# Kernel optimization log

Hardware: AMD Instinct MI355X
Metric: run time of the kernel (lower is better)

## Reference

```python
import jax, jax.numpy as jnp
import numpy as np

IN_DIMS = 4
DEPTH = 4
C = IN_DIMS + 1                     # channels after time augmentation
SIG = sum(C ** k for k in range(1, DEPTH + 1))  # 780
N, T = 64, 1024


def setup_inputs() -> dict:
    key = jax.random.key(0)
    k1, k2, k3, k4, k5 = jax.random.split(key, 5)
    batch = jax.random.normal(k1, (N, T, IN_DIMS), dtype=jnp.float32)
    s_c = 1.0 / np.sqrt(C)
    conv_w = jax.random.normal(k2, (C, C), dtype=jnp.float32) * s_c
    conv_b = jax.random.normal(k3, (C,), dtype=jnp.float32) * s_c
    s_l = 1.0 / np.sqrt(SIG)
    lin_w = jax.random.normal(k4, (SIG, SIG), dtype=jnp.float32) * s_l
    lin_b = jax.random.normal(k5, (SIG,), dtype=jnp.float32) * s_l
    return {"batch": batch, "conv_w": conv_w, "conv_b": conv_b,
            "lin_w": lin_w, "lin_b": lin_b}


def _stream_signature(path):
    """Streamed path signature with zero basepoint.

    path: (n, t, C). Returns (n, t, SIG) where entry t is the signature of
    the piecewise-linear path (0, path[0], ..., path[t]) truncated at DEPTH,
    levels flattened in lexicographic (row-major) order like signatory.
    """
    n = path.shape[0]
    # increments; basepoint=True means first increment is path[:,0] - 0
    dx = jnp.concatenate([path[:, :1, :], path[:, 1:, :] - path[:, :-1, :]], axis=1)
    init = tuple(jnp.zeros((n, C ** k), path.dtype) for k in range(1, DEPTH + 1))

    def step(levels, d):
        # exp(d) in the truncated tensor algebra: e_k = d^{(x)k} / k!
        e = [d]
        for k in range(2, DEPTH + 1):
            e.append((jnp.einsum('na,nb->nab', e[-1], d) / k).reshape(n, -1))
        # Chen: new_k = e_k + S_k + sum_{i=1}^{k-1} S_i (x) e_{k-i}
        new = []
        for k in range(1, DEPTH + 1):
            acc = levels[k - 1] + e[k - 1]
            for i in range(1, k):
                acc = acc + jnp.einsum('na,nb->nab', levels[i - 1], e[k - i - 1]).reshape(n, -1)
            new.append(acc)
        new = tuple(new)
        return new, jnp.concatenate(new, axis=-1)

    _, ys = jax.lax.scan(step, init, jnp.swapaxes(dx, 0, 1))  # ys: (t, n, SIG)
    return jnp.swapaxes(ys, 0, 1)


def reference(batch, conv_w, conv_b, lin_w, lin_b):
    n, t, _ = batch.shape
    # time augmentation: append channel arange(1,T+1)/T
    time = (jnp.arange(1, t + 1, dtype=batch.dtype) / t)[None, :, None]
    a = jnp.concatenate([batch, jnp.broadcast_to(time, (n, t, 1))], axis=-1)  # (n,t,C)
    # kernel-size-1 conv1d == pointwise linear over channels
    b = a @ conv_w.T + conv_b                                                  # (n,t,C)
    c = _stream_signature(b)                                                   # (n,t,SIG)
    # zero out the first stream entry (torch.concat of zeros with c[:,1:,:])
    c = jnp.concatenate([jnp.zeros((n, 1, SIG), c.dtype), c[:, 1:, :]], axis=1)
    return jnp.tanh(c @ lin_w.T + lin_b)
```

## Files before the change

kernel.cpp:

```cpp
#include <hip/hip_runtime.h>
#include <math.h>

#define N_B 64
#define T_LEN 1024
#define IN_D 4
#define CH 5
#define SIG 780
#define KP 800
#define SEG_LEN 16
#define N_SEG 64
#define SC_L1 1.0f
#define SC_L2 0.25f
#define SC_L3 0.0625f
#define SC_L4 0.015625f

typedef _Float16 f16x8 __attribute__((ext_vector_type(8)));
typedef float f32x4 __attribute__((ext_vector_type(4)));

typedef __attribute__((address_space(1))) const void* as1cp;
typedef __attribute__((address_space(3))) void* as3p;

__device__ __forceinline__ float fast_tanh(float x) {
  float ax = fabsf(x);
  float e = __expf(-2.0f * ax);
  float r = (1.0f - e) * __builtin_amdgcn_rcpf(1.0f + e);
  return copysignf(r, x);
}

__global__ __launch_bounds__(256) void conv_kernel(
    const float* __restrict__ batch,
    const float* __restrict__ conv_w,
    const float* __restrict__ conv_b,
    float* __restrict__ b_out) {
  int idx = blockIdx.x * blockDim.x + threadIdx.x;
  if (idx >= N_B * T_LEN) return;
  int t = idx & (T_LEN - 1);
  const float* a = batch + (size_t)idx * IN_D;
  float a0 = a[0], a1 = a[1], a2 = a[2], a3 = a[3];
  float tm = (float)(t + 1) / (float)T_LEN;
  float* o = b_out + (size_t)idx * CH;
#pragma unroll
  for (int j = 0; j < CH; ++j) {
    const float* w = conv_w + j * CH;
    float r = conv_b[j];
    r = fmaf(tm, w[4], r);
    r = fmaf(a3, w[3], r);
    r = fmaf(a2, w[2], r);
    r = fmaf(a1, w[1], r);
    r = fmaf(a0, w[0], r);
    o[j] = r;
  }
}

__global__ __launch_bounds__(320) void seg_kernel(
    const float* __restrict__ batch,
    const float* __restrict__ conv_w,
    const float* __restrict__ conv_b,
    float* __restrict__ P) {
  int s = blockIdx.x;
  int n = blockIdx.y;
  int tid = threadIdx.x;

  __shared__ float S[SIG];
  __shared__ float bc[(SEG_LEN + 1) * CH];
  __shared__ float dsh[SEG_LEN][CH];

  for (int i = tid; i < SIG; i += 320) S[i] = 0.0f;
  if (tid < (SEG_LEN + 1) * CH) {
    int r = s * SEG_LEN - 1 + tid / CH, ch = tid % CH;
    float v = 0.0f;
    if (r >= 0) {
      const float* a = batch + ((size_t)n * T_LEN + r) * IN_D;
      const float* w = conv_w + ch * CH;
      v = conv_b[ch];
      v = fmaf(a[0], w[0], v);
      v = fmaf(a[1], w[1], v);
      v = fmaf(a[2], w[2], v);
      v = fmaf(a[3], w[3], v);
      v = fmaf((float)(r + 1) * (1.0f / T_LEN), w[4], v);
    }
    bc[tid] = v;
  }
  __syncthreads();
  if (tid < SEG_LEN * CH) {
    int j = tid / CH, ch = tid % CH;
    dsh[j][ch] = bc[(j + 1) * CH + ch] - bc[j * CH + ch];
  }

  const int x0 = tid;
  const int x1 = tid + 320;
  const bool has1 = (tid < 305);
  const int a0i = x0 / 125, b0i = (x0 / 25) % 5, c0i = (x0 / 5) % 5, d0i = x0 % 5;
  const int a1i = x1 / 125, b1i = (x1 / 25) % 5, c1i = (x1 / 5) % 5, d1i = x1 % 5;
  const int s2_0 = x0 / 25, s3_0 = x0 / 5;
  const int s2_1 = x1 / 25, s3_1 = x1 / 5;
  const bool hasL3 = (tid < 125);
  const int ya = tid / 25, yb = (tid / 5) % 5, yc = tid % 5;
  const bool hasL2 = (tid < 25);
  const int za = tid / 5, zb = tid % 5;
  const bool hasL1 = (tid < CH);
  __syncthreads();

  for (int j = 0; j < SEG_LEN; ++j) {
    float n4_0, n4_1 = 0.0f, n3 = 0.0f, n2 = 0.0f, n1 = 0.0f;
    {
      float tH = fmaf(0.25f, dsh[j][a0i], S[a0i]);
      tH = fmaf((1.0f / 3.0f) * dsh[j][b0i], tH, S[5 + s2_0]);
      tH = fmaf(0.5f * dsh[j][c0i], tH, S[30 + s3_0]);
      n4_0 = fmaf(dsh[j][d0i], tH, S[155 + x0]);
    }
    if (has1) {
      float tH = fmaf(0.25f, dsh[j][a1i], S[a1i]);
      tH = fmaf((1.0f / 3.0f) * dsh[j][b1i], tH, S[5 + s2_1]);
      tH = fmaf(0.5f * dsh[j][c1i], tH, S[30 + s3_1]);
      n4_1 = fmaf(dsh[j][d1i], tH, S[155 + x1]);
    }
    if (hasL3) {
      float tH = fmaf((1.0f / 3.0f), dsh[j][ya], S[ya]);
      tH = fmaf(0.5f * dsh[j][yb], tH, S[5 + ya * 5 + yb]);
      n3 = fmaf(dsh[j][yc], tH, S[30 + tid]);
    }
    if (hasL2) {
      float tH = fmaf(0.5f, dsh[j][za], S[za]);
      n2 = fmaf(dsh[j][zb], tH, S[5 + tid]);
    }
    if (hasL1) n1 = S[tid] + dsh[j][tid];
    __syncthreads();
    S[155 + x0] = n4_0;
    if (has1) S[155 + x1] = n4_1;
    if (hasL3) S[30 + tid] = n3;
    if (hasL2) S[5 + tid] = n2;
    if (hasL1) S[tid] = n1;
    __syncthreads();
  }

  float* Pr = P + ((size_t)n * N_SEG + s) * SIG;
  for (int i = tid; i < SIG; i += 320) Pr[i] = S[i];
}

__global__ __launch_bounds__(640) void prefix_kernel(float* __restrict__ P) {
  int n = blockIdx.x;
  int tid = threadIdx.x;
  __shared__ float A[SIG];
  __shared__ float Bs[SIG];

  float* Pn = P + (size_t)n * N_SEG * SIG;
  for (int i = tid; i < SIG; i += 640) A[i] = Pn[i];
  int i0 = tid, i1 = tid + 640;
  float r0 = 0.f, r1 = 0.f;
  if (i0 < SIG) r0 = Pn[SIG + i0];
  if (i1 < SIG) r1 = Pn[SIG + i1];

  const int e4 = tid;
  const int q4a = e4 / 125, r125 = e4 % 125, r25 = e4 % 25, r5 = e4 % 5;
  const int e4d5 = e4 / 5, e4d25 = e4 / 25;
  const int e3 = tid;
  const int e3a = e3 / 25, e3r25 = e3 % 25, e3r5 = e3 % 5, e3d5 = e3 / 5;
  const int e2 = tid - 125;
  const int e1 = tid - 150;

  for (int s = 1; s < N_SEG; ++s) {
    if (i0 < SIG) Bs[i0] = r0;
    if (i1 < SIG) Bs[i1] = r1;
    __syncthreads();
    if (s + 1 < N_SEG) {
      const float* Pnx = Pn + (size_t)(s + 1) * SIG;
      if (i0 < SIG) r0 = Pnx[i0];
      if (i1 < SIG) r1 = Pnx[i1];
    }
    float v4 = 0.f, v3 = 0.f, v2 = 0.f, v1 = 0.f;
    if (tid < 625) {
      v4 = A[155 + e4] + Bs[155 + e4];
      v4 = fmaf(A[30 + e4d5], Bs[r5], v4);
      v4 = fmaf(A[5 + e4d25], Bs[5 + r25], v4);
      v4 = fmaf(A[q4a], Bs[30 + r125], v4);
    }
    if (tid < 125) {
      v3 = A[30 + e3] + Bs[30 + e3];
      v3 = fmaf(A[5 + e3d5], Bs[e3r5], v3);
      v3 = fmaf(A[e3a], Bs[5 + e3r25], v3);
    } else if (tid < 150) {
      v2 = A[5 + e2] + Bs[5 + e2];
      v2 = fmaf(A[e2 / 5], Bs[e2 % 5], v2);
    } else if (tid < 155) {
      v1 = A[e1] + Bs[e1];
    }
    __syncthreads();
    float* Po = Pn + (size_t)s * SIG;
    if (tid < 625) { A[155 + e4] = v4; Po[155 + e4] = v4; }
    if (tid < 125) { A[30 + e3] = v3; Po[30 + e3] = v3; }
    else if (tid < 150) { A[5 + e2] = v2; Po[5 + e2] = v2; }
    else if (tid < 155) { A[e1] = v1; Po[e1] = v1; }
  }
}

__global__ __launch_bounds__(320) void emit_kernel(
    const float* __restrict__ batch,
    const float* __restrict__ conv_w,
    const float* __restrict__ conv_b,
    const float* __restrict__ P,
    _Float16* __restrict__ c1,
    _Float16* __restrict__ c2) {
  int s = blockIdx.x;
  int n = blockIdx.y;
  int tid = threadIdx.x;

  __shared__ float S[SIG];
  __shared__ float bc[(SEG_LEN + 1) * CH];
  __shared__ float dsh[SEG_LEN][CH];
  __shared__ __align__(16) _Float16 row1[KP];
  __shared__ __align__(16) _Float16 row2[KP];

  if (s == 0) {
    for (int i = tid; i < SIG; i += 320) S[i] = 0.0f;
  } else {
    const float* Pr = P + ((size_t)n * N_SEG + (s - 1)) * SIG;
    for (int i = tid; i < SIG; i += 320) S[i] = Pr[i];
  }
  if (tid < (SEG_LEN + 1) * CH) {
    int r = s * SEG_LEN - 1 + tid / CH, ch = tid % CH;
    float v = 0.0f;
    if (r >= 0) {
      const float* a = batch + ((size_t)n * T_LEN + r) * IN_D;
      const float* w = conv_w + ch * CH;
      v = conv_b[ch];
      v = fmaf(a[0], w[0], v);
      v = fmaf(a[1], w[1], v);
      v = fmaf(a[2], w[2], v);
      v = fmaf(a[3], w[3], v);
      v = fmaf((float)(r + 1) * (1.0f / T_LEN), w[4], v);
    }
    bc[tid] = v;
  }
  if (tid < KP - SIG) {
    row1[SIG + tid] = (_Float16)0.0f;
    row2[SIG + tid] = (_Float16)0.0f;
  }
  __syncthreads();
  if (tid < SEG_LEN * CH) {
    int j = tid / CH, ch = tid % CH;
    dsh[j][ch] = bc[(j + 1) * CH + ch] - bc[j * CH + ch];
  }

  const int x0 = tid;
  const int x1 = tid + 320;
  const bool has1 = (tid < 305);
  const int a0i = x0 / 125, b0i = (x0 / 25) % 5, c0i = (x0 / 5) % 5, d0i = x0 % 5;
  const int a1i = x1 / 125, b1i = (x1 / 25) % 5, c1i = (x1 / 5) % 5, d1i = x1 % 5;
  const int s2_0 = x0 / 25, s3_0 = x0 / 5;
  const int s2_1 = x1 / 25, s3_1 = x1 / 5;
  const bool hasL3 = (tid < 125);
  const int ya = tid / 25, yb = (tid / 5) % 5, yc = tid % 5;
  const bool hasL2 = (tid < 25);
  const int za = tid / 5, zb = tid % 5;
  const bool hasL1 = (tid < CH);
  __syncthreads();

  for (int j = 0; j < SEG_LEN; ++j) {
    int t = s * SEG_LEN + j;
    float n4_0, n4_1 = 0.0f, n3 = 0.0f, n2 = 0.0f, n1 = 0.0f;
    {
      float tH = fmaf(0.25f, dsh[j][a0i], S[a0i]);
      tH = fmaf((1.0f / 3.0f) * dsh[j][b0i], tH, S[5 + s2_0]);
      tH = fmaf(0.5f * dsh[j][c0i], tH, S[30 + s3_0]);
      n4_0 = fmaf(dsh[j][d0i], tH, S[155 + x0]);
    }
    if (has1) {
      float tH = fmaf(0.25f, dsh[j][a1i], S[a1i]);
      tH = fmaf((1.0f / 3.0f) * dsh[j][b1i], tH, S[5 + s2_1]);
      tH = fmaf(0.5f * dsh[j][c1i], tH, S[30 + s3_1]);
      n4_1 = fmaf(dsh[j][d1i], tH, S[155 + x1]);
    }
    if (hasL3) {
      float tH = fmaf((1.0f / 3.0f), dsh[j][ya], S[ya]);
      tH = fmaf(0.5f * dsh[j][yb], tH, S[5 + ya * 5 + yb]);
      n3 = fmaf(dsh[j][yc], tH, S[30 + tid]);
    }
    if (hasL2) {
      float tH = fmaf(0.5f, dsh[j][za], S[za]);
      n2 = fmaf(dsh[j][zb], tH, S[5 + tid]);
    }
    if (hasL1) n1 = S[tid] + dsh[j][tid];
    __syncthreads();

    S[155 + x0] = n4_0;
    if (has1) S[155 + x1] = n4_1;
    if (hasL3) S[30 + tid] = n3;
    if (hasL2) S[5 + tid] = n2;
    if (hasL1) S[tid] = n1;

    float z = (t == 0) ? 0.0f : 1.0f;
    {
      float v = n4_0 * SC_L4 * z;
      _Float16 h = (_Float16)v;
      row1[155 + x0] = h; row2[155 + x0] = (_Float16)(v - (float)h);
    }
    if (has1) {
      float v = n4_1 * SC_L4 * z;
      _Float16 h = (_Float16)v;
      row1[155 + x1] = h; row2[155 + x1] = (_Float16)(v - (float)h);
    }
    if (hasL3) {
      float v = n3 * SC_L3 * z;
      _Float16 h = (_Float16)v;
      row1[30 + tid] = h; row2[30 + tid] = (_Float16)(v - (float)h);
    }
    if (hasL2) {
      float v = n2 * SC_L2 * z;
      _Float16 h = (_Float16)v;
      row1[5 + tid] = h; row2[5 + tid] = (_Float16)(v - (float)h);
    }
    if (hasL1) {
      float v = n1 * SC_L1 * z;
      _Float16 h = (_Float16)v;
      row1[tid] = h; row2[tid] = (_Float16)(v - (float)h);
    }
    __syncthreads();

    size_t base = ((size_t)n * T_LEN + t) * KP;
    if (tid < 100) {
      *(float4*)(c1 + base + tid * 8) = *(const float4*)&row1[tid * 8];
    } else if (tid < 200) {
      int c = tid - 100;
      *(float4*)(c2 + base + c * 8) = *(const float4*)&row2[c * 8];
    }
  }
}

__global__ __launch_bounds__(256) void wconv_kernel(
    const float* __restrict__ W,
    _Float16* __restrict__ w1,
    _Float16* __restrict__ w2) {
  int idx = blockIdx.x * blockDim.x + threadIdx.x;
  if (idx >= 896 * KP) return;
  int nn = idx / KP, k = idx % KP;
  float v = 0.0f;
  if (nn < SIG && k < SIG) {
    float sc = (k < 5) ? 1.0f : (k < 30) ? 4.0f : (k < 155) ? 16.0f : 64.0f;
    v = W[(size_t)nn * SIG + k] * sc;
  }
  _Float16 h = (_Float16)v;
  w1[idx] = h;
  w2[idx] = (_Float16)(v - (float)h);
}

__global__ __launch_bounds__(256) void gemm_mfma(
    const _Float16* __restrict__ A1p, const _Float16* __restrict__ A2p,
    const _Float16* __restrict__ B1p, const _Float16* __restrict__ B2p,
    const float* __restrict__ bias, float* __restrict__ out) {
  __shared__ _Float16 Al[2][2][128 * 32];
  __shared__ _Float16 Bl[2][2][128 * 32];

  int tid = threadIdx.x;
  int lane = tid & 63, wid = tid >> 6;
  int wm = wid >> 1, wn = wid & 1;
  int m0 = blockIdx.y * 128;
  int n0 = blockIdx.x * 128;

  f32x4 acc[4][4];
#pragma unroll
  for (int i = 0; i < 4; ++i)
#pragma unroll
    for (int j = 0; j < 4; ++j) acc[i][j] = (f32x4){0.f, 0.f, 0.f, 0.f};

  int sr = lane >> 2, scn = lane & 3;
  int swst = (sr ^ (sr >> 2)) & 3;
  int qg = scn ^ swst;
  int fr = lane & 15, fq = lane >> 4;
  int swf = (fr ^ (fr >> 2)) & 3;
  int fchunk = fq ^ swf;

  auto stage = [&](int kb, int buf) {
    int k0 = kb * 32;
#pragma unroll
    for (int i = 0; i < 2; ++i) {
      int rloc = wid * 16 + i * 64 + sr;
      size_t gA = (size_t)(m0 + rloc) * KP + k0 + qg * 8;
      size_t gB = (size_t)(n0 + rloc) * KP + k0 + qg * 8;
      int lb = (wid * 16 + i * 64) * 32;
      __builtin_amdgcn_global_load_lds((as1cp)(A1p + gA), (as3p)(&Al[buf][0][lb]), 16, 0, 0);
      __builtin_amdgcn_global_load_lds((as1cp)(A2p + gA), (as3p)(&Al[buf][1][lb]), 16, 0, 0);
      __builtin_amdgcn_global_load_lds((as1cp)(B1p + gB), (as3p)(&Bl[buf][0][lb]), 16, 0, 0);
      __builtin_amdgcn_global_load_lds((as1cp)(B2p + gB), (as3p)(&Bl[buf][1][lb]), 16, 0, 0);
    }
  };

  stage(0, 0);
  for (int kb = 0; kb < 25; ++kb) {
    int cur = kb & 1;
    __syncthreads();
    f16x8 a1[4], a2[4], b1[4], b2[4];
#pragma unroll
    for (int tm = 0; tm < 4; ++tm) {
      int off = (wm * 64 + tm * 16 + fr) * 32 + fchunk * 8;
      a1[tm] = *(const f16x8*)&Al[cur][0][off];
      a2[tm] = *(const f16x8*)&Al[cur][1][off];
    }
#pragma unroll
    for (int tn = 0; tn < 4; ++tn) {
      int off = (wn * 64 + tn * 16 + fr) * 32 + fchunk * 8;
      b1[tn] = *(const f16x8*)&Bl[cur][0][off];
      b2[tn] = *(const f16x8*)&Bl[cur][1][off];
    }
    if (kb < 24) stage(kb + 1, cur ^ 1);
#pragma unroll
    for (int tm = 0; tm < 4; ++tm)
#pragma unroll
      for (int tn = 0; tn < 4; ++tn) {
        acc[tm][tn] = __builtin_amdgcn_mfma_f32_16x16x32_f16(a1[tm], b1[tn], acc[tm][tn], 0, 0, 0);
        acc[tm][tn] = __builtin_amdgcn_mfma_f32_16x16x32_f16(a1[tm], b2[tn], acc[tm][tn], 0, 0, 0);
        acc[tm][tn] = __builtin_amdgcn_mfma_f32_16x16x32_f16(a2[tm], b1[tn], acc[tm][tn], 0, 0, 0);
      }
  }
  __syncthreads();

  float* ep = (float*)((wid < 2) ? (void*)&Al[0][0][0] : (void*)&Bl[0][0][0]);
  ep += (wid & 1) * 4096;

  float bv[4];
#pragma unroll
  for (int tn = 0; tn < 4; ++tn) {
    int nn = n0 + wn * 64 + tn * 16 + fr;
    bv[tn] = (nn < SIG) ? bias[nn] : 0.0f;
  }
#pragma unroll
  for (int h = 0; h < 2; ++h) {
#pragma unroll
    for (int tm2 = 0; tm2 < 2; ++tm2) {
      int tm = h * 2 + tm2;
#pragma unroll
      for (int tn = 0; tn < 4; ++tn) {
#pragma unroll
        for (int r = 0; r < 4; ++r) {
          int lr = tm2 * 16 + fq * 4 + r;
          int lc = tn * 16 + fr;
          ep[lr * 66 + lc] = fast_tanh(acc[tm][tn][r] + bv[tn]);
        }
      }
    }
#pragma unroll
    for (int p = 0; p < 2; ++p) {
      int lr = lane & 31;
      int ck = (lane >> 5) * 2 + p;
      int gm = m0 + wm * 64 + h * 32 + lr;
      int gc0 = n0 + wn * 64 + ck * 16;
#pragma unroll
      for (int q = 0; q < 4; ++q) {
        int col = gc0 + q * 4;
        if (col + 3 < SIG) {
          *(float4*)(out + (size_t)gm * SIG + col) =
              *(const float4*)&ep[lr * 66 + ck * 16 + q * 4];
        } else if (col < SIG) {
#pragma unroll
          for (int e = 0; e < 4; ++e) {
            int c2 = col + e;
            if (c2 < SIG) out[(size_t)gm * SIG + c2] = ep[lr * 66 + ck * 16 + q * 4 + e];
          }
        }
      }
    }
  }
}

__global__ __launch_bounds__(320) void sig_kernel_fb(
    const float* __restrict__ b_in, float* __restrict__ c_out) {
  int n = blockIdx.x;
  int tid = threadIdx.x;
  __shared__ float S[SIG];
  __shared__ float bc[64 * CH];
  __shared__ float dsh[CH];
  __shared__ float pb[CH];
  for (int i = tid; i < SIG; i += 320) S[i] = 0.0f;
  if (tid < CH) pb[tid] = 0.0f;
  const float* bn = b_in + (size_t)n * T_LEN * CH;
  float* cn = c_out + (size_t)n * T_LEN * SIG;
  const int x0 = tid, x1 = tid + 320;
  const bool has1 = (tid < 305);
  const int a0i = x0 / 125, b0i = (x0 / 25) % 5, c0i = (x0 / 5) % 5, d0i = x0 % 5;
  const int a1i = x1 / 125, b1i = (x1 / 25) % 5, c1i = (x1 / 5) % 5, d1i = x1 % 5;
  const int s2_0 = x0 / 25, s3_0 = x0 / 5, s2_1 = x1 / 25, s3_1 = x1 / 5;
  const bool hasL3 = (tid < 125);
  const int ya = tid / 25, yb = (tid / 5) % 5, yc = tid % 5;
  const bool hasL2 = (tid < 25);
  const int za = tid / 5, zb = tid % 5;
  const bool hasL1 = (tid < CH);
  for (int t = 0; t < T_LEN; ++t) {
    if ((t & 63) == 0) {
      __syncthreads();
      bc[tid] = bn[t * CH + tid];
      __syncthreads();
    }
    if (tid < CH) {
      float cur = bc[(t & 63) * CH + tid];
      dsh[tid] = cur - pb[tid];
      pb[tid] = cur;
    }
    __syncthreads();
    float n4_0, n4_1 = 0.0f, n3 = 0.0f, n2 = 0.0f, n1 = 0.0f;
    {
      float tH = fmaf(0.25f, dsh[a0i], S[a0i]);
      tH = fmaf((1.0f / 3.0f) * dsh[b0i], tH, S[5 + s2_0]);
      tH = fmaf(0.5f * dsh[c0i], tH, S[30 + s3_0]);
      n4_0 = fmaf(dsh[d0i], tH, S[155 + x0]);
    }
    if (has1) {
      float tH = fmaf(0.25f, dsh[a1i], S[a1i]);
      tH = fmaf((1.0f / 3.0f) * dsh[b1i], tH, S[5 + s2_1]);
      tH = fmaf(0.5f * dsh[c1i], tH, S[30 + s3_1]);
      n4_1 = fmaf(dsh[d1i], tH, S[155 + x1]);
    }
    if (hasL3) {
      float tH = fmaf((1.0f / 3.0f), dsh[ya], S[ya]);
      tH = fmaf(0.5f * dsh[yb], tH, S[5 + ya * 5 + yb]);
      n3 = fmaf(dsh[yc], tH, S[30 + tid]);
    }
    if (hasL2) {
      float tH = fmaf(0.5f, dsh[za], S[za]);
      n2 = fmaf(dsh[zb], tH, S[5 + tid]);
    }
    if (hasL1) n1 = S[tid] + dsh[tid];
    __syncthreads();
    S[155 + x0] = n4_0;
    if (has1) S[155 + x1] = n4_1;
    if (hasL3) S[30 + tid] = n3;
    if (hasL2) S[5 + tid] = n2;
    if (hasL1) S[tid] = n1;
    float* crow = cn + (size_t)t * SIG;
    float z = (t == 0) ? 0.0f : 1.0f;
    crow[155 + x0] = n4_0 * z;
    if (has1) crow[155 + x1] = n4_1 * z;
    if (hasL3) crow[30 + tid] = n3 * z;
    if (hasL2) crow[5 + tid] = n2 * z;
    if (hasL1) crow[tid] = n1 * z;
    __syncthreads();
  }
}

#define BM 256
#define BN 64
#define BK 16
__global__ __launch_bounds__(256) void gemm_tanh_fb(
    const float* __restrict__ Cmat, const float* __restrict__ W,
    const float* __restrict__ bias, float* __restrict__ out) {
  __shared__ float As[BK][BM + 4];
  __shared__ float Ws[BK][BN + 4];
  int tid = threadIdx.x;
  int tx = tid & 7, ty = tid >> 3;
  int m0 = blockIdx.x * BM, n0 = blockIdx.y * BN;
  float acc[8][8];
#pragma unroll
  for (int i = 0; i < 8; ++i)
#pragma unroll
    for (int j = 0; j < 8; ++j) acc[i][j] = 0.0f;
  for (int kb = 0; kb < SIG; kb += BK) {
    __syncthreads();
#pragma unroll
    for (int p = 0; p < 4; ++p) {
      int id = tid + p * 256;
      int row = id >> 2, kg = (id & 3) * 4, gk = kb + kg;
      float4 v = make_float4(0.f, 0.f, 0.f, 0.f);
      if (gk < SIG) v = *(const float4*)(Cmat + (size_t)(m0 + row) * SIG + gk);
      As[kg + 0][row] = v.x; As[kg + 1][row] = v.y;
      As[kg + 2][row] = v.z; As[kg + 3][row] = v.w;
    }
    {
      int row = tid >> 2, kg = (tid & 3) * 4, gk = kb + kg, wr = n0 + row;
      float4 v = make_float4(0.f, 0.f, 0.f, 0.f);
      if (gk < SIG && wr < SIG) v = *(const float4*)(W + (size_t)wr * SIG + gk);
      Ws[kg + 0][row] = v.x; Ws[kg + 1][row] = v.y;
      Ws[kg + 2][row] = v.z; Ws[kg + 3][row] = v.w;
    }
    __syncthreads();
#pragma unroll
    for (int k = 0; k < BK; ++k) {
      float af[8], wf[8];
      *(float4*)&af[0] = *(const float4*)&As[k][ty * 8];
      *(float4*)&af[4] = *(const float4*)&As[k][ty * 8 + 4];
      *(float4*)&wf[0] = *(const float4*)&Ws[k][tx * 8];
      *(float4*)&wf[4] = *(const float4*)&Ws[k][tx * 8 + 4];
#pragma unroll
      for (int i = 0; i < 8; ++i)
#pragma unroll
        for (int j = 0; j < 8; ++j) acc[i][j] = fmaf(af[i], wf[j], acc[i][j]);
    }
  }
#pragma unroll
  for (int i = 0; i < 8; ++i) {
    int m = m0 + ty * 8 + i;
    float* orow = out + (size_t)m * SIG;
#pragma unroll
    for (int jj = 0; jj < 8; jj += 4) {
      int col = n0 + tx * 8 + jj;
      if (col < SIG) {
        float4 r;
        r.x = tanhf(acc[i][jj + 0] + bias[col + 0]);
        r.y = tanhf(acc[i][jj + 1] + bias[col + 1]);
        r.z = tanhf(acc[i][jj + 2] + bias[col + 2]);
        r.w = tanhf(acc[i][jj + 3] + bias[col + 3]);
        *(float4*)(orow + col) = r;
      }
    }
  }
}

extern "C" void kernel_launch(void* const* d_in, const int* in_sizes, int n_in,
                              void* d_out, int out_size, void* d_ws, size_t ws_size,
                              hipStream_t stream) {
  const float* batch = (const float*)d_in[0];
  const float* conv_w = (const float*)d_in[1];
  const float* conv_b = (const float*)d_in[2];
  const float* lin_w = (const float*)d_in[3];
  const float* lin_b = (const float*)d_in[4];
  float* out = (float*)d_out;

  const size_t plane_elems = (size_t)N_B * T_LEN * KP;
  const size_t wplane_elems = (size_t)896 * KP;
  const size_t P_elems = (size_t)N_B * N_SEG * SIG;
  const size_t bp_elems = (size_t)N_B * T_LEN * CH;
  const size_t need_big = 2 * plane_elems * sizeof(_Float16) +
                          2 * wplane_elems * sizeof(_Float16) +
                          P_elems * sizeof(float);

  if (ws_size >= need_big) {
    _Float16* c1 = (_Float16*)d_ws;
    _Float16* c2 = c1 + plane_elems;
    _Float16* w1 = c2 + plane_elems;
    _Float16* w2 = w1 + wplane_elems;
    float* P = (float*)(w2 + wplane_elems);

    wconv_kernel<<<dim3((896 * KP + 255) / 256), dim3(256), 0, stream>>>(
        lin_w, w1, w2);
    seg_kernel<<<dim3(N_SEG, N_B), dim3(320), 0, stream>>>(batch, conv_w, conv_b, P);
    prefix_kernel<<<dim3(N_B), dim3(640), 0, stream>>>(P);
    emit_kernel<<<dim3(N_SEG, N_B), dim3(320), 0, stream>>>(
        batch, conv_w, conv_b, P, c1, c2);
    gemm_mfma<<<dim3(7, 512), dim3(256), 0, stream>>>(c1, c2, w1, w2, lin_b, out);
  } else {
    float* b_path = (float*)d_ws;
    float* c_sig = (float*)d_ws + bp_elems;
    conv_kernel<<<dim3((N_B * T_LEN + 255) / 256), dim3(256), 0, stream>>>(
        batch, conv_w, conv_b, b_path);
    sig_kernel_fb<<<dim3(N_B), dim3(320), 0, stream>>>(b_path, c_sig);
    gemm_tanh_fb<<<dim3((N_B * T_LEN) / BM, (SIG + BN - 1) / BN), dim3(256), 0, stream>>>(
        c_sig, lin_w, lin_b, out);
  }
}
```

Before: 714.1 us.

## Restructure split-f16 MFMA GEMM into 256x128 tiles with 3-stage async pipeline

```diff
diff --git a/kernel.cpp b/kernel.cpp
--- a/kernel.cpp
+++ b/kernel.cpp
@@ -19,6 +19,8 @@
 
 typedef __attribute__((address_space(1))) const void* as1cp;
 typedef __attribute__((address_space(3))) void* as3p;
+
+#define VMCNT(n) asm volatile("s_waitcnt vmcnt(" #n ")" ::: "memory")
 
 __device__ __forceinline__ float fast_tanh(float x) {
   float ax = fabsf(x);
@@ -344,18 +346,23 @@
   w2[idx] = (_Float16)(v - (float)h);
 }
 
-__global__ __launch_bounds__(256) void gemm_mfma(
+__global__ __launch_bounds__(512, 2) void gemm_mfma(
     const _Float16* __restrict__ A1p, const _Float16* __restrict__ A2p,
     const _Float16* __restrict__ B1p, const _Float16* __restrict__ B2p,
     const float* __restrict__ bias, float* __restrict__ out) {
-  __shared__ _Float16 Al[2][2][128 * 32];
-  __shared__ _Float16 Bl[2][2][128 * 32];
+  __shared__ _Float16 Al[3][2][256 * 32];
+  __shared__ _Float16 Bl[3][2][128 * 32];
 
   int tid = threadIdx.x;
   int lane = tid & 63, wid = tid >> 6;
   int wm = wid >> 1, wn = wid & 1;
-  int m0 = blockIdx.y * 128;
-  int n0 = blockIdx.x * 128;
+
+  int b = blockIdx.x;
+  int xcd = b & 7, sidx = b >> 3;
+  int mt = (sidx / 7) * 8 + xcd;
+  int nt = sidx % 7;
+  int m0 = mt * 256;
+  int n0 = nt * 128;
 
   f32x4 acc[4][4];
 #pragma unroll
@@ -370,52 +377,84 @@
   int swf = (fr ^ (fr >> 2)) & 3;
   int fchunk = fq ^ swf;
 
-  auto stage = [&](int kb, int buf) {
+  auto stageA = [&](int kb, int buf, int i) {
     int k0 = kb * 32;
-#pragma unroll
-    for (int i = 0; i < 2; ++i) {
-      int rloc = wid * 16 + i * 64 + sr;
-      size_t gA = (size_t)(m0 + rloc) * KP + k0 + qg * 8;
-      size_t gB = (size_t)(n0 + rloc) * KP + k0 + qg * 8;
-      int lb = (wid * 16 + i * 64) * 32;
-      __builtin_amdgcn_global_load_lds((as1cp)(A1p + gA), (as3p)(&Al[buf][0][lb]), 16, 0, 0);
-      __builtin_amdgcn_global_load_lds((as1cp)(A2p + gA), (as3p)(&Al[buf][1][lb]), 16, 0, 0);
-      __builtin_amdgcn_global_load_lds((as1cp)(B1p + gB), (as3p)(&Bl[buf][0][lb]), 16, 0, 0);
-      __builtin_amdgcn_global_load_lds((as1cp)(B2p + gB), (as3p)(&Bl[buf][1][lb]), 16, 0, 0);
-    }
+    int linear = wid * 4 + i;
+    int plane = linear >> 4, grp = linear & 15;
+    size_t g = (size_t)(m0 + grp * 16 + sr) * KP + k0 + qg * 8;
+    const _Float16* src = (plane ? A2p : A1p) + g;
+    __builtin_amdgcn_global_load_lds((as1cp)src, (as3p)(&Al[buf][plane][grp * 512]), 16, 0, 0);
   };
-
-  stage(0, 0);
+  auto stageB = [&](int kb, int buf, int i) {
+    int k0 = kb * 32;
+    int linear = wid * 2 + i;
+    int plane = linear >> 3, grp = linear & 7;
+    size_t g = (size_t)(n0 + grp * 16 + sr) * KP + k0 + qg * 8;
+    const _Float16* src = (plane ? B2p : B1p) + g;
+    __builtin_amdgcn_global_load_lds((as1cp)src, (as3p)(&Bl[buf][plane][grp * 512]), 16, 0, 0);
+  };
+
+#pragma unroll
+  for (int i = 0; i < 4; ++i) stageA(0, 0, i);
+#pragma unroll
+  for (int i = 0; i < 2; ++i) stageB(0, 0, i);
+#pragma unroll
+  for (int i = 0; i < 4; ++i) stageA(1, 1, i);
+#pragma unroll
+  for (int i = 0; i < 2; ++i) stageB(1, 1, i);
+
+  f16x8 b1f[4], b2f[4];
+  int cur = 0;
+#pragma unroll 1
   for (int kb = 0; kb < 25; ++kb) {
-    int cur = kb & 1;
-    __syncthreads();
-    f16x8 a1[4], a2[4], b1[4], b2[4];
-#pragma unroll
-    for (int tm = 0; tm < 4; ++tm) {
-      int off = (wm * 64 + tm * 16 + fr) * 32 + fchunk * 8;
-      a1[tm] = *(const f16x8*)&Al[cur][0][off];
-      a2[tm] = *(const f16x8*)&Al[cur][1][off];
-    }
-#pragma unroll
-    for (int tn = 0; tn < 4; ++tn) {
-      int off = (wn * 64 + tn * 16 + fr) * 32 + fchunk * 8;
-      b1[tn] = *(const f16x8*)&Bl[cur][0][off];
-      b2[tn] = *(const f16x8*)&Bl[cur][1][off];
-    }
-    if (kb < 24) stage(kb + 1, cur ^ 1);
-#pragma unroll
-    for (int tm = 0; tm < 4; ++tm)
-#pragma unroll
-      for (int tn = 0; tn < 4; ++tn) {
-        acc[tm][tn] = __builtin_amdgcn_mfma_f32_16x16x32_f16(a1[tm], b1[tn], acc[tm][tn], 0, 0, 0);
-        acc[tm][tn] = __builtin_amdgcn_mfma_f32_16x16x32_f16(a1[tm], b2[tn], acc[tm][tn], 0, 0, 0);
-        acc[tm][tn] = __builtin_amdgcn_mfma_f32_16x16x32_f16(a2[tm], b1[tn], acc[tm][tn], 0, 0, 0);
+    int nx = cur + 2; if (nx >= 3) nx -= 3;
+    bool pf = (kb + 2 < 25);
+    if (kb < 24) { VMCNT(6); } else { VMCNT(0); }
+    __builtin_amdgcn_s_barrier();
+    __builtin_amdgcn_sched_barrier(0);
+#pragma unroll
+    for (int ph = 0; ph < 2; ++ph) {
+      f16x8 a1f[2], a2f[2];
+      if (ph == 0) {
+#pragma unroll
+        for (int tn = 0; tn < 4; ++tn) {
+          int off = (wn * 64 + tn * 16 + fr) * 32 + fchunk * 8;
+          b1f[tn] = *(const f16x8*)&Bl[cur][0][off];
+          b2f[tn] = *(const f16x8*)&Bl[cur][1][off];
+        }
       }
+#pragma unroll
+      for (int t = 0; t < 2; ++t) {
+        int tm = ph * 2 + t;
+        int off = (wm * 64 + tm * 16 + fr) * 32 + fchunk * 8;
+        a1f[t] = *(const f16x8*)&Al[cur][0][off];
+        a2f[t] = *(const f16x8*)&Al[cur][1][off];
+      }
+      if (pf) {
+        stageA(kb + 2, nx, ph * 2 + 0);
+        stageA(kb + 2, nx, ph * 2 + 1);
+        stageB(kb + 2, nx, ph);
+      }
+      __builtin_amdgcn_s_barrier();
+      __builtin_amdgcn_sched_barrier(0);
+      __builtin_amdgcn_s_setprio(1);
+#pragma unroll
+      for (int t = 0; t < 2; ++t) {
+        int tm = ph * 2 + t;
+#pragma unroll
+        for (int tn = 0; tn < 4; ++tn) {
+          acc[tm][tn] = __builtin_amdgcn_mfma_f32_16x16x32_f16(a1f[t], b1f[tn], acc[tm][tn], 0, 0, 0);
+          acc[tm][tn] = __builtin_amdgcn_mfma_f32_16x16x32_f16(a1f[t], b2f[tn], acc[tm][tn], 0, 0, 0);
+          acc[tm][tn] = __builtin_amdgcn_mfma_f32_16x16x32_f16(a2f[t], b1f[tn], acc[tm][tn], 0, 0, 0);
+        }
+      }
+      __builtin_amdgcn_s_setprio(0);
+    }
+    cur = cur + 1; if (cur >= 3) cur -= 3;
   }
   __syncthreads();
 
-  float* ep = (float*)((wid < 2) ? (void*)&Al[0][0][0] : (void*)&Bl[0][0][0]);
-  ep += (wid & 1) * 4096;
+  float* ep = (float*)(&Al[0][0][0]) + wid * 2112;
 
   float bv[4];
 #pragma unroll
@@ -634,7 +673,7 @@
     prefix_kernel<<<dim3(N_B), dim3(640), 0, stream>>>(P);
     emit_kernel<<<dim3(N_SEG, N_B), dim3(320), 0, stream>>>(
         batch, conv_w, conv_b, P, c1, c2);
-    gemm_mfma<<<dim3(7, 512), dim3(256), 0, stream>>>(c1, c2, w1, w2, lin_b, out);
+    gemm_mfma<<<dim3(1792), dim3(512), 0, stream>>>(c1, c2, w1, w2, lin_b, out);
   } else {
     float* b_path = (float*)d_ws;
     float* c_sig = (float*)d_ws + bp_elems;
```

Result: faster. 662.0 us (-7.3%).
